# Performance work log

Hardware: AMD Instinct MI355X
Metric: run time of the kernel (lower is better)

The kernel has to match this reference:

```python
import jax, jax.numpy as jnp
import numpy as np


def setup_inputs() -> dict:
    key = jax.random.key(0)
    ka, kb = jax.random.split(key)
    a = jax.random.normal(ka, (16384, 3), dtype=jnp.float32)
    b = jax.random.normal(kb, (16384, 3), dtype=jnp.float32)
    return {"a": a, "b": b}


def reference(a, b):
    # Pairwise Euclidean distances via ||a||^2 + ||b||^2 - 2 a.b (avoids [N,M,D] diff tensor).
    a2 = jnp.sum(a * a, axis=-1)            # [N]
    b2 = jnp.sum(b * b, axis=-1)            # [M]
    sq = a2[:, None] + b2[None, :] - 2.0 * jnp.einsum("nd,md->nm", a, b)  # [N,M]
    dist = jnp.sqrt(jnp.maximum(sq, 0.0))
    min_a = jnp.min(dist, axis=1)           # nearest b for each a
    min_b = jnp.min(dist, axis=0)           # nearest a for each b
    return jnp.mean(jnp.concatenate([min_a, min_b]))
```

## Files before the change

kernel.cpp:

```cpp
#include <hip/hip_runtime.h>

typedef unsigned int uint32;
typedef unsigned short ushort16;
typedef __attribute__((ext_vector_type(16))) float f32x16;
typedef __attribute__((ext_vector_type(8)))  short short8;

#define THREADS 256
#define QB 128
#define CH 8
#define JS 8
#define RB 64

__device__ inline ushort16 bf16rn(float x) {
    uint32 u = __float_as_uint(x);
    u += 0x7FFFu + ((u >> 16) & 1u);
    return (ushort16)(u >> 16);
}
__device__ inline float bf2f(ushort16 h) { return __uint_as_float(((uint32)h) << 16); }

__device__ inline void prep_one(const float* __restrict__ P, int np, int i,
                                short8* __restrict__ Qf, short8* __restrict__ Sf,
                                float* __restrict__ a2)
{
    ushort16 qs[16], ss[16];
#pragma unroll
    for (int s = 0; s < 16; ++s) { qs[s] = 0; ss[s] = 0; }
    float w = 0.f;
    if (i < np) {
        float c[3] = {P[3*i], P[3*i+1], P[3*i+2]};
        w = fmaf(c[0], c[0], fmaf(c[1], c[1], c[2]*c[2]));
#pragma unroll
        for (int cc = 0; cc < 3; ++cc) {
            ushort16 h = bf16rn(c[cc]);
            ushort16 m = bf16rn(c[cc] - bf2f(h));
            float bv = -2.f * c[cc];
            ushort16 bh = bf16rn(bv);
            ushort16 bm = bf16rn(bv - bf2f(bh));
            const int b = 4*cc;
            qs[b]=h;  qs[b+1]=h;  qs[b+2]=m;  qs[b+3]=m;
            ss[b]=bh; ss[b+1]=bm; ss[b+2]=bh; ss[b+3]=bm;
        }
        qs[12]=0x3F80; qs[13]=0x3F80; qs[14]=0x3F80;
        ushort16 wh = bf16rn(w);
        float r1 = w - bf2f(wh);
        ushort16 wm = bf16rn(r1);
        ushort16 wl = bf16rn(r1 - bf2f(wm));
        ss[12]=wh; ss[13]=wm; ss[14]=wl;
    } else {
        ss[12] = bf16rn(1e30f);
    }
    a2[i] = w;
    const int row = i & 31, grp = i >> 5;
#pragma unroll
    for (int h = 0; h < 2; ++h) {
        short8 qv, sv;
#pragma unroll
        for (int e = 0; e < 8; ++e) { qv[e] = (short)qs[8*h+e]; sv[e] = (short)ss[8*h+e]; }
        Qf[(size_t)grp*64 + h*32 + row] = qv;
        Sf[(size_t)grp*64 + h*32 + row] = sv;
    }
}

__global__ __launch_bounds__(THREADS) void cd_prep(
    const float* __restrict__ A, int n, int padN,
    const float* __restrict__ B, int m, int padM,
    short8* QfA, short8* SfA, float* a2A,
    short8* QfB, short8* SfB, float* a2B,
    uint32* bits)
{
    const int i = blockIdx.x * THREADS + threadIdx.x;
    if (i < n + m) bits[i] = 0x7F800000u;
    if (i < padN) prep_one(A, n, i, QfA, SfA, a2A);
    if (i < padM) prep_one(B, m, i, QfB, SfB, a2B);
}

__device__ inline float dppmin(float v, int ctrl) {
    float s;
    switch (ctrl) {
        case 0xB1:  s = __int_as_float(__builtin_amdgcn_mov_dpp(__float_as_int(v), 0xB1,  0xf, 0xf, false)); break;
        case 0x4E:  s = __int_as_float(__builtin_amdgcn_mov_dpp(__float_as_int(v), 0x4E,  0xf, 0xf, false)); break;
        case 0x141: s = __int_as_float(__builtin_amdgcn_mov_dpp(__float_as_int(v), 0x141, 0xf, 0xf, false)); break;
        default:    s = __int_as_float(__builtin_amdgcn_mov_dpp(__float_as_int(v), 0x140, 0xf, 0xf, false)); break;
    }
    return fminf(v, s);
}

__global__ __launch_bounds__(THREADS, 4) void cd_mfma(
    const short8* __restrict__ QfA, const short8* __restrict__ SfA,
    const float* __restrict__ a2A, int padN, int n,
    const short8* __restrict__ QfB, const short8* __restrict__ SfB,
    const float* __restrict__ a2B, int padM, int m,
    uint32* __restrict__ bits)
{
    __shared__ short8 sb[2][CH*64];

    const short8* Qf; const short8* Sf; const float* a2; uint32* outb;
    int nq, padQ, padS;
    if (blockIdx.z == 0) { Qf=QfA; a2=a2A; nq=n; padQ=padN; Sf=SfB; padS=padM; outb=bits;   }
    else                 { Qf=QfB; a2=a2B; nq=m; padQ=padM; Sf=SfA; padS=padN; outb=bits+n; }

    if ((int)(blockIdx.x * QB) >= padQ) return;
    const int ntiles = padS >> 5;
    const int tps = ((ntiles + JS*CH - 1) / (JS*CH)) * CH;
    const int t0 = blockIdx.y * tps;
    const int t1 = min(t0 + tps, ntiles);
    if (t0 >= t1) return;

    const int tid = threadIdx.x, lane = tid & 63, wid = tid >> 6;
    const int qbase = blockIdx.x * QB + wid * 32;

    const short8 av = Qf[(size_t)(qbase >> 5) * 64 + lane];

    f32x16 pc;
    {
        const int rb = qbase + 4 * (lane >> 5);
#pragma unroll
        for (int r = 0; r < 16; ++r) pc[r] = a2[rb + (r & 3) + 8 * (r >> 2)];
    }

    float rmin[16];
#pragma unroll
    for (int r = 0; r < 16; ++r) rmin[r] = 1e30f;

    const int nch = (t1 - t0 + CH - 1) / CH;

    {
        const int elems = min(CH, t1 - t0) * 64;
        if (tid       < elems) sb[0][tid      ] = Sf[(size_t)t0*64 + tid      ];
        if (tid + 256 < elems) sb[0][tid + 256] = Sf[(size_t)t0*64 + tid + 256];
    }
    __syncthreads();

    int cur = 0;
    for (int ch = 0; ch < nch; ++ch) {
        const int tb = t0 + ch*CH;
        const int cnt = min(CH, t1 - tb);

        short8 st0, st1;
        bool sv0=false, sv1=false;
        if (ch + 1 < nch) {
            const int nb = tb + CH;
            const int nel = min(CH, t1 - nb) * 64;
            const size_t gb = (size_t)nb * 64;
            if (tid       < nel) { st0 = Sf[gb + tid      ]; sv0 = true; }
            if (tid + 256 < nel) { st1 = Sf[gb + tid + 256]; sv1 = true; }
        }

        int t = 0;
        for (; t + 2 <= cnt; t += 2) {
            const short8 b0 = sb[cur][t*64 + lane];
            const short8 b1 = sb[cur][t*64 + 64 + lane];
            const f32x16 c0 = __builtin_amdgcn_mfma_f32_32x32x16_bf16(av, b0, pc, 0, 0, 0);
            const f32x16 c1 = __builtin_amdgcn_mfma_f32_32x32x16_bf16(av, b1, pc, 0, 0, 0);
#pragma unroll
            for (int r = 0; r < 16; ++r)
                rmin[r] = fminf(fminf(rmin[r], c0[r]), c1[r]);
        }
        if (t < cnt) {
            const short8 b0 = sb[cur][t*64 + lane];
            const f32x16 c0 = __builtin_amdgcn_mfma_f32_32x32x16_bf16(av, b0, pc, 0, 0, 0);
#pragma unroll
            for (int r = 0; r < 16; ++r) rmin[r] = fminf(rmin[r], c0[r]);
        }

        if (ch + 1 < nch) {
            if (sv0) sb[cur^1][tid      ] = st0;
            if (sv1) sb[cur^1][tid + 256] = st1;
        }
        __syncthreads();
        cur ^= 1;
    }

#pragma unroll
    for (int r = 0; r < 16; ++r) {
        float v = rmin[r];
        v = dppmin(v, 0xB1);
        v = dppmin(v, 0x4E);
        v = dppmin(v, 0x141);
        v = dppmin(v, 0x140);
        v = fminf(v, __shfl_xor(v, 16, 64));
        rmin[r] = v;
    }

    if ((lane & 31) == 0) {
        const int rb = qbase + 4 * (lane >> 5);
#pragma unroll
        for (int r = 0; r < 16; ++r) {
            const int qi = rb + (r & 3) + 8 * (r >> 2);
            if (qi < nq) {
                const float sq = fmaxf(rmin[r], 0.f);
                atomicMin(&outb[qi], __float_as_uint(sq));
            }
        }
    }
}

__global__ __launch_bounds__(THREADS) void cd_reduce1(
    const uint32* __restrict__ bits, int count, double* __restrict__ partials)
{
    double s = 0.0;
    for (int i = blockIdx.x * THREADS + threadIdx.x; i < count; i += gridDim.x * THREADS)
        s += (double)sqrtf(__uint_as_float(bits[i]));
#pragma unroll
    for (int off = 32; off; off >>= 1) s += __shfl_down(s, off, 64);
    __shared__ double sw[4];
    const int lane = threadIdx.x & 63, wid = threadIdx.x >> 6;
    if (lane == 0) sw[wid] = s;
    __syncthreads();
    if (threadIdx.x == 0) partials[blockIdx.x] = sw[0] + sw[1] + sw[2] + sw[3];
}

__global__ __launch_bounds__(THREADS) void cd_reduce2(
    const double* __restrict__ partials, int nb, int total, float* __restrict__ out)
{
    double s = 0.0;
    for (int i = threadIdx.x; i < nb; i += THREADS) s += partials[i];
#pragma unroll
    for (int off = 32; off; off >>= 1) s += __shfl_down(s, off, 64);
    __shared__ double sw[4];
    const int lane = threadIdx.x & 63, wid = threadIdx.x >> 6;
    if (lane == 0) sw[wid] = s;
    __syncthreads();
    if (threadIdx.x == 0)
        out[0] = (float)((sw[0] + sw[1] + sw[2] + sw[3]) / (double)total);
}

extern "C" void kernel_launch(void* const* d_in, const int* in_sizes, int n_in,
                              void* d_out, int out_size, void* d_ws, size_t ws_size,
                              hipStream_t stream) {
    const float* a = (const float*)d_in[0];
    const float* b = (const float*)d_in[1];
    const int n = in_sizes[0] / 3;
    const int m = in_sizes[1] / 3;
    const int total = n + m;
    float* out = (float*)d_out;

    const int padN = (n + QB - 1) / QB * QB;
    const int padM = (m + QB - 1) / QB * QB;

    char* wp = (char*)d_ws;
    short8* QfA = (short8*)wp;   wp += (size_t)padN * 64;
    short8* SfA = (short8*)wp;   wp += (size_t)padN * 64;
    float*  a2A = (float*)wp;    wp += (size_t)padN * 4;
    short8* QfB = (short8*)wp;   wp += (size_t)padM * 64;
    short8* SfB = (short8*)wp;   wp += (size_t)padM * 64;
    float*  a2B = (float*)wp;    wp += (size_t)padM * 4;
    uint32* bits = (uint32*)wp;  wp += (size_t)total * 4;
    wp = (char*)(((size_t)wp + 255) & ~(size_t)255);
    double* partials = (double*)wp;

    const int prepElems = max(max(padN, padM), total);
    cd_prep<<<(prepElems + THREADS - 1) / THREADS, THREADS, 0, stream>>>(
        a, n, padN, b, m, padM, QfA, SfA, a2A, QfB, SfB, a2B, bits);

    const int gx = max(padN, padM) / QB;
    dim3 grid(gx, JS, 2);
    cd_mfma<<<grid, THREADS, 0, stream>>>(QfA, SfA, a2A, padN, n,
                                          QfB, SfB, a2B, padM, m, bits);

    cd_reduce1<<<RB, THREADS, 0, stream>>>(bits, total, partials);
    cd_reduce2<<<1, THREADS, 0, stream>>>(partials, RB, total, out);
}
```

Measured before the change: 39.97 us.

## Compute the distance matrix once and take row and column minima together

The kernel previously computed the N×M distance tile twice, once per direction (grid z=2). It now computes it once and takes column minima in-register per MFMA tile, combining them through shared-memory atomicMin. Per-block row and column partial minima go to global buffers, and the reduce kernel takes the minimum across them, which replaces the global atomics. This halves the MFMA work but adds per-tile column reductions, LDS atomics and larger partial buffers for the reduce kernel to scan.

Measured after the change: 43.52 us. 8.9% more time.

```diff
diff --git a/kernel.cpp b/kernel.cpp
--- a/kernel.cpp
+++ b/kernel.cpp
@@ -8,8 +8,8 @@
 #define THREADS 256
 #define QB 128
 #define CH 8
-#define JS 8
-#define RB 64
+#define SLICE 1024
+#define RB 128
 
 __device__ inline ushort16 bf16rn(float x) {
     uint32 u = __float_as_uint(x);
@@ -18,60 +18,73 @@
 }
 __device__ inline float bf2f(ushort16 h) { return __uint_as_float(((uint32)h) << 16); }
 
-__device__ inline void prep_one(const float* __restrict__ P, int np, int i,
-                                short8* __restrict__ Qf, short8* __restrict__ Sf,
-                                float* __restrict__ a2)
-{
-    ushort16 qs[16], ss[16];
-#pragma unroll
-    for (int s = 0; s < 16; ++s) { qs[s] = 0; ss[s] = 0; }
-    float w = 0.f;
-    if (i < np) {
-        float c[3] = {P[3*i], P[3*i+1], P[3*i+2]};
-        w = fmaf(c[0], c[0], fmaf(c[1], c[1], c[2]*c[2]));
-#pragma unroll
-        for (int cc = 0; cc < 3; ++cc) {
-            ushort16 h = bf16rn(c[cc]);
-            ushort16 m = bf16rn(c[cc] - bf2f(h));
-            float bv = -2.f * c[cc];
-            ushort16 bh = bf16rn(bv);
-            ushort16 bm = bf16rn(bv - bf2f(bh));
-            const int b = 4*cc;
-            qs[b]=h;  qs[b+1]=h;  qs[b+2]=m;  qs[b+3]=m;
-            ss[b]=bh; ss[b+1]=bm; ss[b+2]=bh; ss[b+3]=bm;
-        }
-        qs[12]=0x3F80; qs[13]=0x3F80; qs[14]=0x3F80;
-        ushort16 wh = bf16rn(w);
-        float r1 = w - bf2f(wh);
-        ushort16 wm = bf16rn(r1);
-        ushort16 wl = bf16rn(r1 - bf2f(wm));
-        ss[12]=wh; ss[13]=wm; ss[14]=wl;
-    } else {
-        ss[12] = bf16rn(1e30f);
-    }
-    a2[i] = w;
-    const int row = i & 31, grp = i >> 5;
-#pragma unroll
-    for (int h = 0; h < 2; ++h) {
-        short8 qv, sv;
-#pragma unroll
-        for (int e = 0; e < 8; ++e) { qv[e] = (short)qs[8*h+e]; sv[e] = (short)ss[8*h+e]; }
-        Qf[(size_t)grp*64 + h*32 + row] = qv;
-        Sf[(size_t)grp*64 + h*32 + row] = sv;
-    }
-}
-
 __global__ __launch_bounds__(THREADS) void cd_prep(
     const float* __restrict__ A, int n, int padN,
     const float* __restrict__ B, int m, int padM,
-    short8* QfA, short8* SfA, float* a2A,
-    short8* QfB, short8* SfB, float* a2B,
-    uint32* bits)
+    short8* __restrict__ Qf, float* __restrict__ a2,
+    short8* __restrict__ Sf)
 {
     const int i = blockIdx.x * THREADS + threadIdx.x;
-    if (i < n + m) bits[i] = 0x7F800000u;
-    if (i < padN) prep_one(A, n, i, QfA, SfA, a2A);
-    if (i < padM) prep_one(B, m, i, QfB, SfB, a2B);
+
+    if (i < padN) {
+        ushort16 qs[16];
+#pragma unroll
+        for (int s = 0; s < 16; ++s) qs[s] = 0;
+        float w = 1e30f;
+        if (i < n) {
+            float c[3] = {A[3*i], A[3*i+1], A[3*i+2]};
+            w = fmaf(c[0], c[0], fmaf(c[1], c[1], c[2]*c[2]));
+#pragma unroll
+            for (int cc = 0; cc < 3; ++cc) {
+                ushort16 h = bf16rn(c[cc]);
+                ushort16 md = bf16rn(c[cc] - bf2f(h));
+                const int b = 4*cc;
+                qs[b]=h; qs[b+1]=h; qs[b+2]=md; qs[b+3]=md;
+            }
+            qs[12]=0x3F80; qs[13]=0x3F80; qs[14]=0x3F80;
+        }
+        a2[i] = w;
+        const int row = i & 31, grp = i >> 5;
+#pragma unroll
+        for (int h = 0; h < 2; ++h) {
+            short8 qv;
+#pragma unroll
+            for (int e = 0; e < 8; ++e) qv[e] = (short)qs[8*h+e];
+            Qf[(size_t)grp*64 + h*32 + row] = qv;
+        }
+    }
+    if (i < padM) {
+        ushort16 ss[16];
+#pragma unroll
+        for (int s = 0; s < 16; ++s) ss[s] = 0;
+        if (i < m) {
+            float c[3] = {B[3*i], B[3*i+1], B[3*i+2]};
+            float w = fmaf(c[0], c[0], fmaf(c[1], c[1], c[2]*c[2]));
+#pragma unroll
+            for (int cc = 0; cc < 3; ++cc) {
+                float bv = -2.f * c[cc];
+                ushort16 bh = bf16rn(bv);
+                ushort16 bm = bf16rn(bv - bf2f(bh));
+                const int b = 4*cc;
+                ss[b]=bh; ss[b+1]=bm; ss[b+2]=bh; ss[b+3]=bm;
+            }
+            ushort16 wh = bf16rn(w);
+            float r1 = w - bf2f(wh);
+            ushort16 wm = bf16rn(r1);
+            ushort16 wl = bf16rn(r1 - bf2f(wm));
+            ss[12]=wh; ss[13]=wm; ss[14]=wl;
+        } else {
+            ss[12] = bf16rn(1e30f);
+        }
+        const int row = i & 31, grp = i >> 5;
+#pragma unroll
+        for (int h = 0; h < 2; ++h) {
+            short8 sv;
+#pragma unroll
+            for (int e = 0; e < 8; ++e) sv[e] = (short)ss[8*h+e];
+            Sf[(size_t)grp*64 + h*32 + row] = sv;
+        }
+    }
 }
 
 __device__ inline float dppmin(float v, int ctrl) {
@@ -85,29 +98,28 @@
     return fminf(v, s);
 }
 
+__device__ inline float tmin16(const f32x16& c) {
+    float a0 = fminf(fminf(c[0], c[1]), c[2]);
+    float a1 = fminf(fminf(c[3], c[4]), c[5]);
+    float a2_ = fminf(fminf(c[6], c[7]), c[8]);
+    float a3 = fminf(fminf(c[9], c[10]), c[11]);
+    float a4 = fminf(fminf(c[12], c[13]), c[14]);
+    float b0 = fminf(fminf(a0, a1), c[15]);
+    float b1 = fminf(fminf(a2_, a3), a4);
+    return fminf(b0, b1);
+}
+
 __global__ __launch_bounds__(THREADS, 4) void cd_mfma(
-    const short8* __restrict__ QfA, const short8* __restrict__ SfA,
-    const float* __restrict__ a2A, int padN, int n,
-    const short8* __restrict__ QfB, const short8* __restrict__ SfB,
-    const float* __restrict__ a2B, int padM, int m,
-    uint32* __restrict__ bits)
+    const short8* __restrict__ Qf, const float* __restrict__ a2, int padN,
+    const short8* __restrict__ Sf, int padM,
+    float* __restrict__ Pr, float* __restrict__ Pc)
 {
     __shared__ short8 sb[2][CH*64];
-
-    const short8* Qf; const short8* Sf; const float* a2; uint32* outb;
-    int nq, padQ, padS;
-    if (blockIdx.z == 0) { Qf=QfA; a2=a2A; nq=n; padQ=padN; Sf=SfB; padS=padM; outb=bits;   }
-    else                 { Qf=QfB; a2=a2B; nq=m; padQ=padM; Sf=SfA; padS=padN; outb=bits+n; }
-
-    if ((int)(blockIdx.x * QB) >= padQ) return;
-    const int ntiles = padS >> 5;
-    const int tps = ((ntiles + JS*CH - 1) / (JS*CH)) * CH;
-    const int t0 = blockIdx.y * tps;
-    const int t1 = min(t0 + tps, ntiles);
-    if (t0 >= t1) return;
-
+    __shared__ uint32 cmin[SLICE];
+
+    const int ib = blockIdx.x, js = blockIdx.y;
     const int tid = threadIdx.x, lane = tid & 63, wid = tid >> 6;
-    const int qbase = blockIdx.x * QB + wid * 32;
+    const int qbase = ib * QB + wid * 32;
 
     const short8 av = Qf[(size_t)(qbase >> 5) * 64 + lane];
 
@@ -122,32 +134,29 @@
 #pragma unroll
     for (int r = 0; r < 16; ++r) rmin[r] = 1e30f;
 
-    const int nch = (t1 - t0 + CH - 1) / CH;
-
-    {
-        const int elems = min(CH, t1 - t0) * 64;
-        if (tid       < elems) sb[0][tid      ] = Sf[(size_t)t0*64 + tid      ];
-        if (tid + 256 < elems) sb[0][tid + 256] = Sf[(size_t)t0*64 + tid + 256];
-    }
+#pragma unroll
+    for (int u = 0; u < SLICE / THREADS; ++u)
+        cmin[u * THREADS + tid] = 0x7F800000u;
+
+    const int t0 = js * (SLICE / 32);
+    sb[0][tid]       = Sf[(size_t)t0 * 64 + tid];
+    sb[0][tid + 256] = Sf[(size_t)t0 * 64 + tid + 256];
     __syncthreads();
 
+    const int col = lane & 31;
     int cur = 0;
-    for (int ch = 0; ch < nch; ++ch) {
-        const int tb = t0 + ch*CH;
-        const int cnt = min(CH, t1 - tb);
-
+#pragma unroll
+    for (int ch = 0; ch < 4; ++ch) {
         short8 st0, st1;
-        bool sv0=false, sv1=false;
-        if (ch + 1 < nch) {
-            const int nb = tb + CH;
-            const int nel = min(CH, t1 - nb) * 64;
-            const size_t gb = (size_t)nb * 64;
-            if (tid       < nel) { st0 = Sf[gb + tid      ]; sv0 = true; }
-            if (tid + 256 < nel) { st1 = Sf[gb + tid + 256]; sv1 = true; }
-        }
-
-        int t = 0;
-        for (; t + 2 <= cnt; t += 2) {
+        const bool pf = (ch + 1 < 4);
+        if (pf) {
+            const size_t gb = (size_t)(t0 + (ch + 1) * CH) * 64;
+            st0 = Sf[gb + tid];
+            st1 = Sf[gb + tid + 256];
+        }
+
+#pragma unroll
+        for (int t = 0; t < CH; t += 2) {
             const short8 b0 = sb[cur][t*64 + lane];
             const short8 b1 = sb[cur][t*64 + 64 + lane];
             const f32x16 c0 = __builtin_amdgcn_mfma_f32_32x32x16_bf16(av, b0, pc, 0, 0, 0);
@@ -155,17 +164,15 @@
 #pragma unroll
             for (int r = 0; r < 16; ++r)
                 rmin[r] = fminf(fminf(rmin[r], c0[r]), c1[r]);
-        }
-        if (t < cnt) {
-            const short8 b0 = sb[cur][t*64 + lane];
-            const f32x16 c0 = __builtin_amdgcn_mfma_f32_32x32x16_bf16(av, b0, pc, 0, 0, 0);
-#pragma unroll
-            for (int r = 0; r < 16; ++r) rmin[r] = fminf(rmin[r], c0[r]);
-        }
-
-        if (ch + 1 < nch) {
-            if (sv0) sb[cur^1][tid      ] = st0;
-            if (sv1) sb[cur^1][tid + 256] = st1;
+            const float m0 = fmaxf(tmin16(c0), 0.f);
+            const float m1 = fmaxf(tmin16(c1), 0.f);
+            atomicMin(&cmin[(ch*CH + t)     * 32 + col], __float_as_uint(m0));
+            atomicMin(&cmin[(ch*CH + t + 1) * 32 + col], __float_as_uint(m1));
+        }
+
+        if (pf) {
+            sb[cur ^ 1][tid]       = st0;
+            sb[cur ^ 1][tid + 256] = st1;
         }
         __syncthreads();
         cur ^= 1;
@@ -181,26 +188,41 @@
         v = fminf(v, __shfl_xor(v, 16, 64));
         rmin[r] = v;
     }
-
     if ((lane & 31) == 0) {
         const int rb = qbase + 4 * (lane >> 5);
-#pragma unroll
-        for (int r = 0; r < 16; ++r) {
-            const int qi = rb + (r & 3) + 8 * (r >> 2);
-            if (qi < nq) {
-                const float sq = fmaxf(rmin[r], 0.f);
-                atomicMin(&outb[qi], __float_as_uint(sq));
-            }
-        }
-    }
+        float* prow = Pr + (size_t)js * padN;
+#pragma unroll
+        for (int r = 0; r < 16; ++r)
+            prow[rb + (r & 3) + 8 * (r >> 2)] = fmaxf(rmin[r], 0.f);
+    }
+
+    float* pcol = Pc + (size_t)ib * padM + (size_t)js * SLICE;
+#pragma unroll
+    for (int u = 0; u < SLICE / THREADS; ++u)
+        pcol[u * THREADS + tid] = __uint_as_float(cmin[u * THREADS + tid]);
 }
 
 __global__ __launch_bounds__(THREADS) void cd_reduce1(
-    const uint32* __restrict__ bits, int count, double* __restrict__ partials)
-{
+    const float* __restrict__ Pr, int padN, int n, int nJS,
+    const float* __restrict__ Pc, int padM, int m, int gx,
+    double* __restrict__ partials)
+{
+    const int total = n + m;
     double s = 0.0;
-    for (int i = blockIdx.x * THREADS + threadIdx.x; i < count; i += gridDim.x * THREADS)
-        s += (double)sqrtf(__uint_as_float(bits[i]));
+    for (int q = blockIdx.x * THREADS + threadIdx.x; q < total; q += gridDim.x * THREADS) {
+        float v;
+        if (q < n) {
+            v = Pr[q];
+#pragma unroll 4
+            for (int r = 1; r < nJS; ++r) v = fminf(v, Pr[(size_t)r * padN + q]);
+        } else {
+            const int j = q - n;
+            v = Pc[j];
+#pragma unroll 4
+            for (int r = 1; r < gx; ++r) v = fminf(v, Pc[(size_t)r * padM + j]);
+        }
+        s += (double)sqrtf(v);
+    }
 #pragma unroll
     for (int off = 32; off; off >>= 1) s += __shfl_down(s, off, 64);
     __shared__ double sw[4];
@@ -236,28 +258,26 @@
     float* out = (float*)d_out;
 
     const int padN = (n + QB - 1) / QB * QB;
-    const int padM = (m + QB - 1) / QB * QB;
+    const int padM = (m + SLICE - 1) / SLICE * SLICE;
+    const int gx  = padN / QB;
+    const int nJS = padM / SLICE;
 
     char* wp = (char*)d_ws;
-    short8* QfA = (short8*)wp;   wp += (size_t)padN * 64;
-    short8* SfA = (short8*)wp;   wp += (size_t)padN * 64;
-    float*  a2A = (float*)wp;    wp += (size_t)padN * 4;
-    short8* QfB = (short8*)wp;   wp += (size_t)padM * 64;
-    short8* SfB = (short8*)wp;   wp += (size_t)padM * 64;
-    float*  a2B = (float*)wp;    wp += (size_t)padM * 4;
-    uint32* bits = (uint32*)wp;  wp += (size_t)total * 4;
+    short8* Qf = (short8*)wp;    wp += (size_t)padN * 64;
+    float*  a2 = (float*)wp;     wp += (size_t)padN * 4;
+    short8* Sf = (short8*)wp;    wp += (size_t)padM * 64;
+    float*  Pr = (float*)wp;     wp += (size_t)nJS * padN * 4;
+    float*  Pc = (float*)wp;     wp += (size_t)gx * padM * 4;
     wp = (char*)(((size_t)wp + 255) & ~(size_t)255);
     double* partials = (double*)wp;
 
-    const int prepElems = max(max(padN, padM), total);
+    const int prepElems = max(padN, padM);
     cd_prep<<<(prepElems + THREADS - 1) / THREADS, THREADS, 0, stream>>>(
-        a, n, padN, b, m, padM, QfA, SfA, a2A, QfB, SfB, a2B, bits);
-
-    const int gx = max(padN, padM) / QB;
-    dim3 grid(gx, JS, 2);
-    cd_mfma<<<grid, THREADS, 0, stream>>>(QfA, SfA, a2A, padN, n,
-                                          QfB, SfB, a2B, padM, m, bits);
-
-    cd_reduce1<<<RB, THREADS, 0, stream>>>(bits, total, partials);
+        a, n, padN, b, m, padM, Qf, a2, Sf);
+
+    dim3 grid(gx, nJS);
+    cd_mfma<<<grid, THREADS, 0, stream>>>(Qf, a2, padN, Sf, padM, Pr, Pc);
+
+    cd_reduce1<<<RB, THREADS, 0, stream>>>(Pr, padN, n, nJS, Pc, padM, m, gx, partials);
     cd_reduce2<<<1, THREADS, 0, stream>>>(partials, RB, total, out);
 }
```
